# Performance work log

Hardware: AMD Instinct MI355X
Metric: run time of the kernel (lower is better)

Reference implementation:

```python
import jax, jax.numpy as jnp
import numpy as np
import math

ALPHA = 1.8
RGB_FROM_HED = jnp.array([[0.65, 0.7, 0.29],
                          [0.07, 0.99, 0.11],
                          [0.27, 0.57, 0.78]], dtype=jnp.float32)
HED_FROM_RGB = jnp.linalg.inv(RGB_FROM_HED)
COEFFS = jnp.array([0.2125, 0.7154, 0.0721], dtype=jnp.float32)
LOG_ADJUST = math.log(1e-6)                      # negative constant
ADJUST_CAL = 10.0 ** (-math.e ** (1.0 / ALPHA))  # ~0.01802
THRESH_FOD = 0.15
COS_EPS = 1e-8


def compute_od(img):
    """img: [B,H,W,3] RGB in [0,1]. Returns (flat_FOD [B,H*W], avg [B])."""
    rgb = jnp.maximum(img, 1e-6)
    # separate_stains: log(rgb)/log(1e-6) @ hed_from_rgb, clamped at 0
    stains = jnp.maximum(
        jnp.einsum('bhwc,cd->bhwd', jnp.log(rgb) / LOG_ADJUST, HED_FROM_RGB), 0.0)
    d = stains[..., 2]  # DAB channel
    # combine_stains with only channel 2 nonzero:
    #   log_rgb = -((0,0,d) * -log_adjust) @ rgb_from_hed = log_adjust * d * rgb_from_hed[2]
    log_rgb = LOG_ADJUST * d[..., None] * RGB_FROM_HED[2]          # [B,H,W,3]
    rgb_d = jnp.clip(jnp.exp(log_rgb), 0.0, 1.0)
    grey = jnp.clip(rgb_d @ COEFFS, 0.0, 1.0)                       # [B,H,W]
    # FOD = log10(1/(grey+cal)) clamped at 0, then ** alpha
    fod = jnp.maximum(-jnp.log10(grey + ADJUST_CAL), 0.0) ** ALPHA  # [B,H,W]
    fod_relu = jnp.where(fod < THRESH_FOD, 0.0, fod)
    B = img.shape[0]
    flat = fod.reshape(B, -1)            # [B, H*W]
    avg = jnp.sum(fod_relu, axis=(1, 2)) # [B]
    return flat, avg


def gram_cosine(flat):
    """flat: [B,N] -> [1,B,B] pairwise cosine similarity (fused Gram form)."""
    norm = jnp.linalg.norm(flat, axis=1, keepdims=True)
    vn = flat / jnp.maximum(norm, COS_EPS)
    return (vn @ vn.T)[None]


def setup_inputs() -> dict:
    key = jax.random.key(0)
    ks = jax.random.split(key, 6)
    B, H, W = 32, 512, 512
    return {
        'src': jax.random.uniform(ks[0], (B, 3, H, W), dtype=jnp.float32),
        'tgt': jax.random.uniform(ks[1], (B, 3, H, W), dtype=jnp.float32),
        'gen': jax.random.uniform(ks[2], (B, 3, H, W), dtype=jnp.float32),
        'src_feats': jax.random.normal(ks[3], (B, 256, 32, 32), dtype=jnp.float32),
        'tgt_feats': jax.random.normal(ks[4], (B, 256, 32, 32), dtype=jnp.float32),
        'gen_feats': jax.random.normal(ks[5], (B, 256, 32, 32), dtype=jnp.float32),
    }


def reference(src, tgt, gen, src_feats, tgt_feats, gen_feats):
    inp_od, inp_avg = compute_od(jnp.transpose(tgt, (0, 2, 3, 1)))
    out_od, out_avg = compute_od(jnp.transpose(gen, (0, 2, 3, 1)))
    src_matrix = jax.lax.stop_gradient(gram_cosine(inp_od))  # .detach() in torch
    tgt_matrix = gram_cosine(out_od)
    loss = jnp.mean(jnp.abs(src_matrix - tgt_matrix))        # F.l1_loss
    hw = src.shape[2] * src.shape[3]
    loss = loss + jnp.mean((inp_avg - out_avg) ** 2) / float(hw) ** 2  # MSE term
    return loss
```

## Files before the change

### kernel.cpp

```cpp
#include <hip/hip_runtime.h>
#include <cmath>


#define HW    262144
#define CHW   (3*HW)
#define NIMG  32
#define CPB   512
#define GRIDX (HW / CPB)
#define NREP  8

constexpr double M00=0.65, M01=0.70, M02=0.29;
constexpr double M10=0.07, M11=0.99, M12=0.11;
constexpr double M20=0.27, M21=0.57, M22=0.78;
constexpr double DETM = M00*(M11*M22-M12*M21) - M01*(M10*M22-M12*M20)
                      + M02*(M10*M21-M11*M20);
constexpr double H0d =  (M01*M12 - M02*M11) / DETM;
constexpr double H1d = -(M00*M12 - M02*M10) / DETM;
constexpr double H2d =  (M00*M11 - M01*M10) / DETM;

#define H0 ((float)H0d)
#define H1 ((float)H1d)
#define H2 ((float)H2d)

__device__ __forceinline__ float fod1(float r, float g, float b, float cal,
                                      float& racc) {
  float lr = __log2f(fmaxf(r, 1e-6f));
  float lg = __log2f(fmaxf(g, 1e-6f));
  float lb = __log2f(fmaxf(b, 1e-6f));
  float t2 = fminf(lr*H0 + lg*H1 + lb*H2, 0.0f);
  float e0 = exp2f(t2 * 0.27f);
  float e1 = exp2f(t2 * 0.57f);
  float e2 = exp2f(t2 * 0.78f);
  float grey = fminf(e0*0.2125f + e1*0.7154f + e2*0.0721f, 1.0f);
  float x = fmaxf(-0.30102999566398120f * __log2f(grey + cal), 0.0f);
  float f = exp2f(1.8f * __log2f(x));
  racc += (f < 0.15f) ? 0.0f : f;
  return f;
}

__global__ __launch_bounds__(256, 4)
void od_gram_kernel(const float* __restrict__ tgt, const float* __restrict__ gen,
                    float* __restrict__ ws, float cal) {
  const float* img = blockIdx.y ? gen : tgt;
  const int rep = blockIdx.x & (NREP - 1);
  float* gram = ws + (rep << 11) + (blockIdx.y << 10);
  float* avgv = ws + 16384 + (rep << 6) + (blockIdx.y << 5);

  __shared__ float F[NIMG * 256];

  const int t  = threadIdx.x;
  const int wv = t >> 6;
  const int ln = t & 63;

  float acc[4][4];
  #pragma unroll
  for (int r = 0; r < 4; ++r)
    #pragma unroll
    for (int c = 0; c < 4; ++c) acc[r][c] = 0.0f;
  float avgp[8];
  #pragma unroll
  for (int r = 0; r < 8; ++r) avgp[r] = 0.0f;

  const int i0  = (ln >> 3) << 2;
  const int j0  = (ln & 7) << 2;
  const int swi = ln >> 3;
  const int swj = ln & 7;

  const int col0 = blockIdx.x * CPB;

  for (int tile = 0; tile < CPB / 256; ++tile) {
    const int k0 = col0 + (tile << 8);

    #pragma unroll 2
    for (int r = 0; r < 8; ++r) {
      const int b = (wv << 3) + r;
      const float* base = img + b * CHW + k0 + (ln << 2);
      float4 Rv = *(const float4*)(base);
      float4 Gv = *(const float4*)(base + HW);
      float4 Bv = *(const float4*)(base + 2 * HW);
      float4 fo;
      fo.x = fod1(Rv.x, Gv.x, Bv.x, cal, avgp[r]);
      fo.y = fod1(Rv.y, Gv.y, Bv.y, cal, avgp[r]);
      fo.z = fod1(Rv.z, Gv.z, Bv.z, cal, avgp[r]);
      fo.w = fod1(Rv.w, Gv.w, Bv.w, cal, avgp[r]);
      const int sw = (b >> 2) & 7;
      *(float4*)&F[(b << 8) + ((ln ^ sw) << 2)] = fo;
    }
    __syncthreads();

    #pragma unroll 2
    for (int gg = 0; gg < 16; ++gg) {
      const int gq = (wv << 4) + gg;
      float4 av[4];
      #pragma unroll
      for (int r = 0; r < 4; ++r)
        av[r] = *(const float4*)&F[((i0 + r) << 8) + ((gq ^ swi) << 2)];
      #pragma unroll
      for (int c = 0; c < 4; ++c) {
        float4 bv = *(const float4*)&F[((j0 + c) << 8) + ((gq ^ swj) << 2)];
        #pragma unroll
        for (int r = 0; r < 4; ++r)
          acc[r][c] += av[r].x * bv.x + av[r].y * bv.y +
                       av[r].z * bv.z + av[r].w * bv.w;
      }
    }
    __syncthreads();
  }

  #pragma unroll
  for (int r = 0; r < 8; ++r) {
    float v = avgp[r];
    #pragma unroll
    for (int off = 32; off; off >>= 1) v += __shfl_down(v, off, 64);
    if (ln == 0) atomicAdd(&avgv[(wv << 3) + r], v);
  }

  {
    const int base = t << 4;
    #pragma unroll
    for (int r = 0; r < 4; ++r)
      #pragma unroll
      for (int c = 0; c < 4; ++c)
        F[base + (r << 2) + c] = acc[r][c];
    __syncthreads();
    for (int e = t; e < 1024; e += 256) {
      const int i = e >> 5, j = e & 31;
      const int tij = ((i >> 2) << 3) + (j >> 2);
      const int idx = ((i & 3) << 2) + (j & 3);
      float sm = 0.0f;
      #pragma unroll
      for (int w2 = 0; w2 < 4; ++w2)
        sm += F[(((w2 << 6) + tij) << 4) + idx];
      atomicAdd(&gram[e], sm);
    }
  }
}

__global__ __launch_bounds__(256)
void finalize_kernel(const float* __restrict__ ws, float* __restrict__ out) {
  __shared__ float G[2048];
  __shared__ float A[64];
  __shared__ float nrm[64];
  __shared__ float wred[8];
  const int t = threadIdx.x;

  for (int e = t; e < 2048; e += 256) {
    float s = 0.0f;
    #pragma unroll
    for (int r = 0; r < NREP; ++r) s += ws[(r << 11) + e];
    G[e] = s;
  }
  if (t < 64) {
    float s = 0.0f;
    #pragma unroll
    for (int r = 0; r < NREP; ++r) s += ws[16384 + (r << 6) + t];
    A[t] = s;
  }
  __syncthreads();

  if (t < 64) {
    const int tensor = t >> 5, i = t & 31;
    nrm[t] = fmaxf(sqrtf(G[(tensor << 10) + i * 33]), 1e-8f);
  }
  __syncthreads();

  float s1 = 0.0f;
  for (int e = t; e < 1024; e += 256) {
    const int i = e >> 5, j = e & 31;
    const float ct = G[e]        / (nrm[i]      * nrm[j]);
    const float cg = G[1024 + e] / (nrm[32 + i] * nrm[32 + j]);
    s1 += fabsf(ct - cg);
  }
  float s2 = 0.0f;
  if (t < 32) {
    const float d = A[t] - A[32 + t];
    s2 = d * d;
  }
  #pragma unroll
  for (int off = 32; off; off >>= 1) {
    s1 += __shfl_down(s1, off, 64);
    s2 += __shfl_down(s2, off, 64);
  }
  if ((t & 63) == 0) { wred[t >> 6] = s1; wred[4 + (t >> 6)] = s2; }
  __syncthreads();
  if (t == 0) {
    const float a = wred[0] + wred[1] + wred[2] + wred[3];
    const float b = wred[4] + wred[5] + wred[6] + wred[7];
    const double hw2 = 262144.0 * 262144.0;
    out[0] = (float)((double)a / 1024.0 + ((double)b / 32.0) / hw2);
  }
}

extern "C" void kernel_launch(void* const* d_in, const int* in_sizes, int n_in,
                              void* d_out, int out_size, void* d_ws, size_t ws_size,
                              hipStream_t stream) {
  (void)in_sizes; (void)n_in; (void)out_size; (void)ws_size;
  const float* tgt = (const float*)d_in[1];
  const float* gen = (const float*)d_in[2];
  float* out = (float*)d_out;
  float* ws  = (float*)d_ws;

  hipMemsetAsync(d_ws, 0, 16896 * sizeof(float), stream);

  const float cal = (float)pow(10.0, -exp(1.0 / 1.8));

  dim3 grid(GRIDX, 2);
  od_gram_kernel<<<grid, 256, 0, stream>>>(tgt, gen, ws, cal);
  finalize_kernel<<<1, 256, 0, stream>>>(ws, out);
}
```

Before: 322.3 us.

## Compute Gram tile with bf16 MFMA and double-buffered shared tiles

The FOD values are stored in shared memory as bf16 instead of fp32. The per-thread 4x4 scalar FMA Gram accumulation is replaced by the 32x32x16 bf16 MFMA instruction, with A and B both set to the same fragment. The shared buffer is double-buffered so one of the per-tile barriers can be removed. This cuts the VALU work for the 32x32 Gram product, but bf16 rounding of the FOD values lowers the precision of the cosine matrix.

```diff
diff --git a/kernel.cpp b/kernel.cpp
--- a/kernel.cpp
+++ b/kernel.cpp
@@ -8,6 +8,10 @@
 #define CPB   512
 #define GRIDX (HW / CPB)
 #define NREP  8
+
+typedef __attribute__((ext_vector_type(4)))  __bf16 bf16x4;
+typedef __attribute__((ext_vector_type(8)))  __bf16 bf16x8;
+typedef __attribute__((ext_vector_type(16))) float  f32x16;
 
 constexpr double M00=0.65, M01=0.70, M02=0.29;
 constexpr double M10=0.07, M11=0.99, M12=0.11;
@@ -46,30 +50,24 @@
   float* gram = ws + (rep << 11) + (blockIdx.y << 10);
   float* avgv = ws + 16384 + (rep << 6) + (blockIdx.y << 5);
 
-  __shared__ float F[NIMG * 256];
+  __shared__ __bf16 F[2][NIMG * 256];
 
   const int t  = threadIdx.x;
   const int wv = t >> 6;
   const int ln = t & 63;
 
-  float acc[4][4];
+  f32x16 acc;
   #pragma unroll
-  for (int r = 0; r < 4; ++r)
-    #pragma unroll
-    for (int c = 0; c < 4; ++c) acc[r][c] = 0.0f;
+  for (int r = 0; r < 16; ++r) acc[r] = 0.0f;
   float avgp[8];
   #pragma unroll
   for (int r = 0; r < 8; ++r) avgp[r] = 0.0f;
-
-  const int i0  = (ln >> 3) << 2;
-  const int j0  = (ln & 7) << 2;
-  const int swi = ln >> 3;
-  const int swj = ln & 7;
 
   const int col0 = blockIdx.x * CPB;
 
   for (int tile = 0; tile < CPB / 256; ++tile) {
     const int k0 = col0 + (tile << 8);
+    __bf16* Fb = F[tile & 1];
 
     #pragma unroll 2
     for (int r = 0; r < 8; ++r) {
@@ -78,34 +76,26 @@
       float4 Rv = *(const float4*)(base);
       float4 Gv = *(const float4*)(base + HW);
       float4 Bv = *(const float4*)(base + 2 * HW);
-      float4 fo;
-      fo.x = fod1(Rv.x, Gv.x, Bv.x, cal, avgp[r]);
-      fo.y = fod1(Rv.y, Gv.y, Bv.y, cal, avgp[r]);
-      fo.z = fod1(Rv.z, Gv.z, Bv.z, cal, avgp[r]);
-      fo.w = fod1(Rv.w, Gv.w, Bv.w, cal, avgp[r]);
-      const int sw = (b >> 2) & 7;
-      *(float4*)&F[(b << 8) + ((ln ^ sw) << 2)] = fo;
+      bf16x4 fo;
+      fo[0] = (__bf16)fod1(Rv.x, Gv.x, Bv.x, cal, avgp[r]);
+      fo[1] = (__bf16)fod1(Rv.y, Gv.y, Bv.y, cal, avgp[r]);
+      fo[2] = (__bf16)fod1(Rv.z, Gv.z, Bv.z, cal, avgp[r]);
+      fo[3] = (__bf16)fod1(Rv.w, Gv.w, Bv.w, cal, avgp[r]);
+      const int idx = (b << 8) + (((ln << 2)) ^ ((b & 7) << 3));
+      *(bf16x4*)&Fb[idx] = fo;
     }
     __syncthreads();
 
-    #pragma unroll 2
-    for (int gg = 0; gg < 16; ++gg) {
-      const int gq = (wv << 4) + gg;
-      float4 av[4];
-      #pragma unroll
-      for (int r = 0; r < 4; ++r)
-        av[r] = *(const float4*)&F[((i0 + r) << 8) + ((gq ^ swi) << 2)];
-      #pragma unroll
-      for (int c = 0; c < 4; ++c) {
-        float4 bv = *(const float4*)&F[((j0 + c) << 8) + ((gq ^ swj) << 2)];
-        #pragma unroll
-        for (int r = 0; r < 4; ++r)
-          acc[r][c] += av[r].x * bv.x + av[r].y * bv.y +
-                       av[r].z * bv.z + av[r].w * bv.w;
-      }
+    #pragma unroll
+    for (int c = 0; c < 4; ++c) {
+      const int kc = (wv << 2) + c;
+      const int o  = (kc << 4) + ((ln >> 5) << 3);
+      const int ridx = ((ln & 31) << 8) + (o ^ ((ln & 7) << 3));
+      bf16x8 a = *(const bf16x8*)&F[tile & 1][ridx];
+      acc = __builtin_amdgcn_mfma_f32_32x32x16_bf16(a, a, acc, 0, 0, 0);
     }
-    __syncthreads();
   }
+  __syncthreads();
 
   #pragma unroll
   for (int r = 0; r < 8; ++r) {
@@ -116,21 +106,18 @@
   }
 
   {
-    const int base = t << 4;
+    float* S = (float*)F;
     #pragma unroll
-    for (int r = 0; r < 4; ++r)
-      #pragma unroll
-      for (int c = 0; c < 4; ++c)
-        F[base + (r << 2) + c] = acc[r][c];
+    for (int r = 0; r < 16; ++r) S[(t << 4) + r] = acc[r];
     __syncthreads();
     for (int e = t; e < 1024; e += 256) {
       const int i = e >> 5, j = e & 31;
-      const int tij = ((i >> 2) << 3) + (j >> 2);
-      const int idx = ((i & 3) << 2) + (j & 3);
+      const int reg  = (i & 3) | ((i >> 3) << 2);
+      const int lane = j | (((i >> 2) & 1) << 5);
       float sm = 0.0f;
       #pragma unroll
       for (int w2 = 0; w2 < 4; ++w2)
-        sm += F[(((w2 << 6) + tij) << 4) + idx];
+        sm += S[(((w2 << 6) + lane) << 4) + reg];
       atomicAdd(&gram[e], sm);
     }
   }
```

New measurement: 318.9 us. About the same (-1.1%).
